# Kernel tuning notes

Hardware: AMD Instinct MI355X
Metric: run time of the kernel (lower is better)

The kernel has to match this reference:

```python
import jax, jax.numpy as jnp
import numpy as np

B, C, T = 16, 129, 2000
NF, ED, K = 40, 64, 16

def setup_inputs() -> dict:
    key = jax.random.key(0)
    ks = iter(jax.random.split(key, 48))
    def n(shape, s=0.05):
        return jax.random.normal(next(ks), shape, jnp.float32) * s
    inp = {
        'x': jax.random.normal(next(ks), (B, C, T), jnp.float32),
        # temporal conv (1,25) pad (0,12) + BN (inference running stats)
        'tconv_w': n((NF, 1, 1, 25)), 'tconv_b': jnp.zeros((NF,)),
        'tbn_g': jnp.ones((NF,)), 'tbn_b': jnp.zeros((NF,)), 'tbn_m': n((NF,)), 'tbn_v': jnp.ones((NF,)),
        # spatial conv (C,1) + BN
        'sconv_w': n((NF, NF, C, 1)), 'sconv_b': jnp.zeros((NF,)),
        'sbn_g': jnp.ones((NF,)), 'sbn_b': jnp.zeros((NF,)), 'sbn_m': n((NF,)), 'sbn_v': jnp.ones((NF,)),
        # separable: depthwise (1,15) pad (0,7), pointwise 1x1 -> 2*NF, BN
        'dw_w': n((NF, 1, 1, 15)), 'dw_b': jnp.zeros((NF,)),
        'pw_w': n((2 * NF, NF, 1, 1)), 'pw_b': jnp.zeros((2 * NF,)),
        'pbn_g': jnp.ones((2 * NF,)), 'pbn_b': jnp.zeros((2 * NF,)), 'pbn_m': n((2 * NF,)), 'pbn_v': jnp.ones((2 * NF,)),
        # projection 2*NF -> ED
        'proj_w': n((ED, 2 * NF)), 'proj_b': jnp.zeros((ED,)),
        # ENN cell 0 (input ED)
        'wx0': n((K, ED)), 'L0': jnp.eye(K, dtype=jnp.float32) + 0.1 * n((K, K), 1.0),
        'll0': jnp.asarray(np.log(0.1), jnp.float32), 'b0': jnp.zeros((K,)),
        'ln0_g': jnp.ones((K,)), 'ln0_b': jnp.zeros((K,)),
        # ENN cell 1 (input K)
        'wx1': n((K, K)), 'L1': jnp.eye(K, dtype=jnp.float32) + 0.1 * n((K, K), 1.0),
        'll1': jnp.asarray(np.log(0.1), jnp.float32), 'b1': jnp.zeros((K,)),
        'ln1_g': jnp.ones((K,)), 'ln1_b': jnp.zeros((K,)),
        # collapse
        'wq_w': n((K, K)), 'wq_b': jnp.zeros((K,)), 'log_temp': jnp.asarray(0.0, jnp.float32),
    }
    return inp

def _conv(x, w, b, pad, groups=1):
    y = jax.lax.conv_general_dilated(
        x, w, window_strides=(1, 1), padding=pad,
        dimension_numbers=('NCHW', 'OIHW', 'NCHW'), feature_group_count=groups)
    return y + b[None, :, None, None]

def _bn(x, g, b, m, v, eps=1e-5):
    inv = g / jnp.sqrt(v + eps)
    return x * inv[None, :, None, None] + (b - m * inv)[None, :, None, None]

def _cell(x, h, Wx, L, ll, b, g, be, eps=1e-5):
    E = L @ L.T  # PSD entanglement matrix [K,K]
    pre = x @ Wx.T + h @ E.T - jnp.exp(ll) * h + b
    mu = pre.mean(-1, keepdims=True)
    var = pre.var(-1, keepdims=True)
    pre = (pre - mu) / jnp.sqrt(var + eps) * g + be
    return jnp.tanh(pre)

def _forward(x, tconv_w, tconv_b, tbn_g, tbn_b, tbn_m, tbn_v,
             sconv_w, sconv_b, sbn_g, sbn_b, sbn_m, sbn_v,
             dw_w, dw_b, pw_w, pw_b, pbn_g, pbn_b, pbn_m, pbn_v,
             proj_w, proj_b,
             wx0, L0, ll0, b0, ln0_g, ln0_b,
             wx1, L1, ll1, b1, ln1_g, ln1_b,
             wq_w, wq_b, log_temp):
    # ---- SpatialCNN front-end (BN in inference mode, dropout=identity) ----
    o = x[:, None, :, :]                                        # [B,1,C,T]
    o = _conv(o, tconv_w, tconv_b, ((0, 0), (12, 12)))          # [B,NF,C,T]
    o = jax.nn.elu(_bn(o, tbn_g, tbn_b, tbn_m, tbn_v))
    o = _conv(o, sconv_w, sconv_b, ((0, 0), (0, 0)))            # [B,NF,1,T]
    o = jax.nn.elu(_bn(o, sbn_g, sbn_b, sbn_m, sbn_v))
    o = _conv(o, dw_w, dw_b, ((0, 0), (7, 7)), groups=NF)       # depthwise
    o = _conv(o, pw_w, pw_b, ((0, 0), (0, 0)))                  # [B,2NF,1,T]
    o = jax.nn.elu(_bn(o, pbn_g, pbn_b, pbn_m, pbn_v))
    Bn, Ch, _, Tt = o.shape
    o = o.reshape(Bn, Ch, Tt // 4, 4).mean(-1)                  # AvgPool (1,4) -> [B,2NF,T']
    feats = o.transpose(0, 2, 1) @ proj_w.T + proj_b            # [B,T',ED]
    # ---- Entangled RNN over T' steps (lax.scan) ----
    h_init = (jnp.zeros((Bn, K), feats.dtype), jnp.zeros((Bn, K), feats.dtype))
    def step(carry, xt):
        h0, h1 = carry
        h0 = _cell(xt, h0, wx0, L0, ll0, b0, ln0_g, ln0_b)
        h1 = _cell(h0, h1, wx1, L1, ll1, b1, ln1_g, ln1_b)
        return (h0, h1), None
    (h0, h1), _ = jax.lax.scan(step, h_init, feats.transpose(1, 0, 2))
    Z = h1                                                       # [B,K]
    # ---- Collapse attention ----
    q = Z @ wq_w.T + wq_b
    scores = jnp.sum(q * Z, axis=-1, keepdims=True)              # [B,1]
    alpha = jax.nn.softmax(scores / jnp.exp(log_temp), axis=-1)  # [B,1]
    return Z, alpha

def reference(x, tconv_w, tconv_b, tbn_g, tbn_b, tbn_m, tbn_v,
              sconv_w, sconv_b, sbn_g, sbn_b, sbn_m, sbn_v,
              dw_w, dw_b, pw_w, pw_b, pbn_g, pbn_b, pbn_m, pbn_v,
              proj_w, proj_b,
              wx0, L0, ll0, b0, ln0_g, ln0_b,
              wx1, L1, ll1, b1, ln1_g, ln1_b,
              wq_w, wq_b, log_temp):
    return _forward(x, tconv_w, tconv_b, tbn_g, tbn_b, tbn_m, tbn_v,
                    sconv_w, sconv_b, sbn_g, sbn_b, sbn_m, sbn_v,
                    dw_w, dw_b, pw_w, pw_b, pbn_g, pbn_b, pbn_m, pbn_v,
                    proj_w, proj_b,
                    wx0, L0, ll0, b0, ln0_g, ln0_b,
                    wx1, L1, ll1, b1, ln1_g, ln1_b,
                    wq_w, wq_b, log_temp)
```

## Files before the change

kernel.cpp:

```cpp
#include <hip/hip_runtime.h>
#include <math.h>

#define B_ 16
#define C_ 129
#define T_ 2000
#define NF_ 40
#define ED_ 64
#define K_ 16
#define TP_ 500

#define OFF_SB2 1040
#define OFF_PWC 1088
#define OFF_PB2 4288
#define OFF_WP  4368
#define OFF_BP  5648
#define OFF_M0  5664
#define OFF_M1  5920
#define OFF_W1A 6224
#define OFF_W2U 8192
#define OFF_XP  1495040
#define OFF_S2R 1623040

typedef __attribute__((ext_vector_type(8))) short s8v;
typedef __attribute__((ext_vector_type(4))) float f4v;

#define XROW 292

__device__ __forceinline__ float elu_f(float x) {
    return x > 0.f ? x : (__expf(x) - 1.f);
}
__device__ __forceinline__ float tanh2_f(float a2) {
    return fmaf(-2.f, __builtin_amdgcn_rcpf(__expf(a2) + 1.f), 1.f);
}
__device__ __forceinline__ unsigned bfr(float v) {
    return (__float_as_uint(v) + 0x8000u) >> 16;
}

#define DPPF(v, ctrl) __int_as_float(__builtin_amdgcn_update_dpp( \
    0, __float_as_int(v), (ctrl), 0xF, 0xF, false))

#define RSUM16(s) do {                     \
    s += DPPF(s, 0x128);                   \
    s += DPPF(s, 0x124);                   \
    s += DPPF(s, 0x122);                   \
    s += DPPF(s, 0x121);                   \
} while (0)

#define RDLANE(v, L) __int_as_float(__builtin_amdgcn_readlane(__float_as_int(v), (L)))

struct P0 {
    const float *tconv_w, *tconv_b, *tbn_g, *tbn_b, *tbn_m, *tbn_v;
    const float *sconv_b, *sbn_g, *sbn_b, *sbn_m, *sbn_v;
    const float *pw_w, *pw_b, *pbn_g, *pbn_b, *pbn_m, *pbn_v;
    const float *proj_w, *proj_b, *wx0, *b0, *L0, *ll0, *L1, *ll1;
    const float *sconv_w;
    float* ws;
};

__global__ __launch_bounds__(256) void k0_all(P0 p) {
    const int tid = threadIdx.x;
    float* ws = p.ws;
    const float eps = 1e-5f;

    if (blockIdx.x < 1250) {
        const int i = blockIdx.x * 256 + tid;
        if (i < 320000)
            ((float4*)(ws + OFF_S2R))[i] = make_float4(0.f, 0.f, 0.f, 0.f);
        return;
    }
    if (blockIdx.x < 1444) {
        const int e = (blockIdx.x - 1250) * 256 + tid;
        if (e >= C_ * 3 * 2 * 64) return;
        unsigned short* w2b = (unsigned short*)(ws + OFF_W2U);
        const int c = e / 384;
        int r = e - c * 384;
        const int mt = r >> 7; r &= 127;
        const int kc = r >> 6;
        const int lane = r & 63;
        const int g = mt * 16 + (lane & 15);
        const float sinv = (g < NF_) ? p.sbn_g[g] * rsqrtf(p.sbn_v[g] + 1e-5f) : 0.f;
        unsigned short o[8];
#pragma unroll
        for (int j = 0; j < 8; ++j) {
            const int f = kc * 32 + (lane >> 4) * 8 + j;
            float v = 0.f;
            if (g < NF_ && f < NF_) v = p.sconv_w[g * (NF_ * C_) + f * C_ + c] * sinv;
            o[j] = (unsigned short)bfr(v);
        }
        unsigned short* dst = w2b + (size_t)e * 8;
#pragma unroll
        for (int j = 0; j < 8; ++j) dst[j] = o[j];
        return;
    }

    const int gtid = (blockIdx.x - 1444) * 256 + tid;
    const int stride = 8 * 256;
    for (int e = gtid; e < 192; e += stride) {
        const int mt = e >> 6, L = e & 63;
        const int f = mt * 16 + (L & 15);
        float inv = 0.f, bias = 0.f;
        if (f < NF_) {
            inv = p.tbn_g[f] / sqrtf(p.tbn_v[f] + eps);
            bias = p.tconv_b[f] * inv + p.tbn_b[f] - p.tbn_m[f] * inv;
        }
        unsigned short* dst = ((unsigned short*)(ws + OFF_W1A)) + e * 8;
#pragma unroll
        for (int j = 0; j < 8; ++j) {
            const int k = (L >> 4) * 8 + j;
            float v = 0.f;
            if (f < NF_) {
                if (k < 25) v = p.tconv_w[f * 25 + k] * inv;
                else if (k == 25) v = bias;
            }
            dst[j] = (unsigned short)bfr(v);
        }
    }
    for (int f = gtid; f < NF_; f += stride) {
        const float sinv = p.sbn_g[f] / sqrtf(p.sbn_v[f] + eps);
        ws[OFF_SB2 + f] = p.sconv_b[f] * sinv + p.sbn_b[f] - p.sbn_m[f] * sinv;
    }
    for (int e = gtid; e < 3200; e += stride) {
        const int g = e / 40;
        const float pinv = p.pbn_g[g] / sqrtf(p.pbn_v[g] + eps);
        ws[OFF_PWC + e] = p.pw_w[e] * pinv;
    }
    for (int g = gtid; g < 80; g += stride) {
        const float pinv = p.pbn_g[g] / sqrtf(p.pbn_v[g] + eps);
        ws[OFF_PB2 + g] = p.pw_b[g] * pinv + p.pbn_b[g] - p.pbn_m[g] * pinv;
    }
    for (int e = gtid; e < 1280; e += stride) {
        const int k = e / 80, g = e - k * 80;
        float a = 0.f;
        for (int ee = 0; ee < ED_; ++ee)
            a = fmaf(p.wx0[k * ED_ + ee], p.proj_w[ee * 80 + g], a);
        ws[OFF_WP + e] = a;
    }
    for (int k = gtid; k < K_; k += stride) {
        float a = p.b0[k];
        for (int ee = 0; ee < ED_; ++ee)
            a = fmaf(p.wx0[k * ED_ + ee], p.proj_b[ee], a);
        ws[OFF_BP + k] = a;
    }
    for (int e = gtid; e < 256; e += stride) {
        const int k = e >> 4, j = e & 15;
        float a0 = 0.f, a1 = 0.f;
        for (int i = 0; i < 16; ++i) {
            a0 = fmaf(p.L0[k * 16 + i], p.L0[j * 16 + i], a0);
            a1 = fmaf(p.L1[k * 16 + i], p.L1[j * 16 + i], a1);
        }
        if (k == j) { a0 -= expf(p.ll0[0]); a1 -= expf(p.ll1[0]); }
        ws[OFF_M0 + e] = a0;
        ws[OFF_M1 + e] = a1;
    }
}

__global__ __launch_bounds__(256, 4) void k1_mfma(
    const float* __restrict__ x, const unsigned short* __restrict__ w1a,
    const unsigned short* __restrict__ w2b, float* __restrict__ s2raw) {
    __shared__ float xs[17 * XROW];
    __shared__ unsigned int vsI[2048];

    const int tid = threadIdx.x;
    const int split = blockIdx.x & 7;
    const int tile = (blockIdx.x >> 3) & 7;
    const int b = blockIdx.x >> 6;
    const int c0 = (split * C_) >> 3;
    const int c1 = ((split + 1) * C_) >> 3;
    const int cc = c1 - c0;
    const int t0 = tile << 8;
    const int w = tid >> 6;
    const int lane = tid & 63;
    const int n = lane & 15;
    const int q = lane >> 4;
    const int qh = q >> 1;
    const int q1_2 = (q & 1) * 2;
    const bool q3 = (q == 3);
    const int wb = w << 9;
    const int w64 = w << 6;
    const int ln8 = n + q * 8;

    for (int i = tid; i < 2048; i += 256) vsI[i] = 0u;
    for (int e = tid; e < cc * XROW; e += 256) {
        const int cl = e / XROW;
        const int i = e - cl * XROW;
        const int t = t0 - 12 + i;
        float v = 0.f;
        if ((unsigned)t < (unsigned)T_) v = x[(b * C_ + c0 + cl) * T_ + t];
        xs[e] = v;
    }
    __syncthreads();

    const s8v* w1a8 = (const s8v*)w1a;
    s8v wA[3];
#pragma unroll
    for (int mt = 0; mt < 3; ++mt) wA[mt] = w1a8[mt * 64 + lane];

    f4v acc[4][3];
#pragma unroll
    for (int nt = 0; nt < 4; ++nt)
#pragma unroll
        for (int mt = 0; mt < 3; ++mt) acc[nt][mt] = (f4v)0.f;

    const s8v* w2b8 = (const s8v*)w2b;
    const f4v z4 = (f4v)0.f;

    for (int cl = 0; cl < cc; ++cl) {
        const int c = c0 + cl;
        s8v af[3][2];
#pragma unroll
        for (int mt = 0; mt < 3; ++mt)
#pragma unroll
            for (int kc = 0; kc < 2; ++kc)
                af[mt][kc] = w2b8[((c * 3 + mt) * 2 + kc) * 64 + lane];

        const float* xrow = &xs[cl * XROW + w64 + ln8];

#pragma unroll
        for (int nt = 0; nt < 4; ++nt) {
            float bx[8];
#pragma unroll
            for (int j = 0; j < 8; ++j) bx[j] = xrow[nt * 16 + j];
            if (q3) bx[1] = 1.0f;
            unsigned pw_[4];
#pragma unroll
            for (int jj = 0; jj < 4; ++jj)
                pw_[jj] = bfr(bx[2 * jj]) |
                    ((__float_as_uint(bx[2 * jj + 1]) + 0x8000u) & 0xFFFF0000u);
            const s8v bh = *(const s8v*)pw_;
#pragma unroll
            for (int mt = 0; mt < 3; ++mt) {
                const f4v vT = __builtin_amdgcn_mfma_f32_16x16x32_bf16(
                    wA[mt], bh, z4, 0, 0, 0);
                const float e0 = elu_f(vT[0]);
                const float e1 = elu_f(vT[1]);
                const float e2 = elu_f(vT[2]);
                const float e3 = elu_f(vT[3]);
                const unsigned lo = bfr(e0) |
                    ((__float_as_uint(e1) + 0x8000u) & 0xFFFF0000u);
                const unsigned hi = bfr(e2) |
                    ((__float_as_uint(e3) + 0x8000u) & 0xFFFF0000u);
                const int base = wb + ((2 * mt + qh) << 6) + (n << 2) + q1_2;
                vsI[base] = lo;
                vsI[base + 1] = hi;
            }
            __builtin_amdgcn_wave_barrier();
            const s8v b0 = *(const s8v*)&vsI[wb + (q << 6) + (n << 2)];
            const s8v b1 = *(const s8v*)&vsI[wb + ((4 + q) << 6) + (n << 2)];
#pragma unroll
            for (int mt = 0; mt < 3; ++mt) {
                acc[nt][mt] = __builtin_amdgcn_mfma_f32_16x16x32_bf16(
                    af[mt][0], b0, acc[nt][mt], 0, 0, 0);
                acc[nt][mt] = __builtin_amdgcn_mfma_f32_16x16x32_bf16(
                    af[mt][1], b1, acc[nt][mt], 0, 0, 0);
            }
            __builtin_amdgcn_wave_barrier();
        }
    }

#pragma unroll
    for (int nt = 0; nt < 4; ++nt) {
        const int t = t0 + w * 64 + nt * 16 + n;
        if (t >= T_) continue;
#pragma unroll
        for (int mt = 0; mt < 3; ++mt) {
#pragma unroll
            for (int r = 0; r < 4; ++r) {
                const int g = mt * 16 + q * 4 + r;
                if (g < NF_)
                    atomicAdd(&s2raw[(b * NF_ + g) * T_ + t], acc[nt][mt][r]);
            }
        }
    }
}

__global__ __launch_bounds__(256) void k2_dwpw(
    const float* __restrict__ s2raw, const float* __restrict__ sb2,
    const float* __restrict__ dw_w, const float* __restrict__ dw_b,
    const float* __restrict__ pwc, const float* __restrict__ pb2,
    const float* __restrict__ WP, const float* __restrict__ bp,
    float* __restrict__ xp) {
    __shared__ float st[NF_ * 114];
    __shared__ float dwo[NF_ * 100];
    __shared__ float dwwl[NF_ * 15];
    __shared__ float dwbl[NF_];
    __shared__ float pwcl[80 * 40];
    __shared__ float pb2l[80];
    __shared__ float WPl[K_ * 80];
    __shared__ float bpl[K_];
    __shared__ float po[80 * 25];
    const int tid = threadIdx.x;
    const int b = blockIdx.x / 20;
    const int tp0 = (blockIdx.x % 20) * 25;
    const int tbase = tp0 * 4 - 7;
    for (int e = tid; e < NF_ * 114; e += 256) {
        const int f = e / 114;
        const int i = e - f * 114;
        const int t = tbase + i;
        float v = 0.f;
        if ((unsigned)t < (unsigned)T_)
            v = elu_f(s2raw[(b * NF_ + f) * T_ + t] + sb2[f]);
        st[e] = v;
    }
    for (int e = tid; e < 600; e += 256) dwwl[e] = dw_w[e];
    for (int e = tid; e < 3200; e += 256) pwcl[e] = pwc[e];
    for (int e = tid; e < 1280; e += 256) WPl[e] = WP[e];
    if (tid < NF_) dwbl[tid] = dw_b[tid];
    if (tid < 80) pb2l[tid] = pb2[tid];
    if (tid < K_) bpl[tid] = bp[tid];
    __syncthreads();
    for (int e = tid; e < 4000; e += 256) {
        const int f = e / 100;
        const int tq = e - f * 100;
        float a = dwbl[f];
#pragma unroll
        for (int kk = 0; kk < 15; ++kk)
            a = fmaf(dwwl[f * 15 + kk], st[f * 114 + tq + kk], a);
        dwo[e] = a;
    }
    __syncthreads();
    for (int e = tid; e < 2000; e += 256) {
        const int g = e / 25;
        const int tp = e - g * 25;
        float sum = 0.f;
#pragma unroll
        for (int dt = 0; dt < 4; ++dt) {
            float a = pb2l[g];
            for (int f = 0; f < NF_; ++f)
                a = fmaf(pwcl[g * 40 + f], dwo[f * 100 + tp * 4 + dt], a);
            sum += elu_f(a);
        }
        po[e] = sum * 0.25f;
    }
    __syncthreads();
    for (int e = tid; e < 400; e += 256) {
        const int tp = e >> 4;
        const int k = e & 15;
        float a = bpl[k];
        for (int g = 0; g < 80; ++g)
            a = fmaf(WPl[k * 80 + g], po[g * 25 + tp], a);
        xp[(b * TP_ + tp0 + tp) * K_ + k] = a;
    }
}

#define SCAN_STEP(I, S) do {                                              \
    float sH0[16], sH1[16];                                               \
    _Pragma("unroll")                                                     \
    for (int j = 0; j < 16; ++j) {                                        \
        sH0[j] = RDLANE(vA, 32 + j);                                      \
        sH1[j] = RDLANE(vA, j);                                           \
    }                                                                     \
    float a0 = 0.f, a1 = 0.f, c0 = 0.f, c1 = 0.f;                         \
    _Pragma("unroll")                                                     \
    for (int j = 0; j < 16; j += 2) {                                     \
        a0 = fmaf(WA[j],     sH0[j],     a0);                             \
        a1 = fmaf(WA[j + 1], sH0[j + 1], a1);                             \
        c0 = fmaf(WB[j],     sH1[j],     c0);                             \
        c1 = fmaf(WB[j + 1], sH1[j + 1], c1);                             \
    }                                                                     \
    const float xv = xn[S];                                               \
    int tf = (I) + 5; if (tf > TP_ - 1) tf = TP_ - 1;                     \
    xn[S] = xpb[tf * K_];                                                 \
    const float cadd = lower ? b1r : xv;                                  \
    const float pre = ((a0 + a1) + (c0 + c1)) + cadd;                     \
    float s1 = pre, s2 = pre * pre;                                       \
    RSUM16(s1);                                                           \
    RSUM16(s2);                                                           \
    const float mu = s1 * 0.0625f;                                        \
    const float var = fmaf(s2, 0.0625f, -mu * mu);                        \
    vA = tanh2_f(fmaf((pre - mu) * rsqrtf(var + 1e-5f), gg, bb));         \
} while (0)

__global__ __launch_bounds__(64, 1) void k3_scan(
    const float* __restrict__ xp, const float* __restrict__ M0,
    const float* __restrict__ M1, const float* __restrict__ wx1,
    const float* __restrict__ b1, const float* __restrict__ ln0_g,
    const float* __restrict__ ln0_b, const float* __restrict__ ln1_g,
    const float* __restrict__ ln1_b, float* __restrict__ out) {
    const int lane = threadIdx.x;
    const int k = lane & 15;
    const bool lower = lane < 32;
    const int b = blockIdx.x;

    float WA[16], WB[16];
#pragma unroll
    for (int j = 0; j < 16; ++j) {
        const float m0 = M0[k * 16 + j];
        const float m1 = M1[k * 16 + j];
        const float wx = wx1[k * 16 + j];
        WA[j] = lower ? wx : m0;
        WB[j] = lower ? m1 : 0.f;
    }
    const float b1r = b1[k];
    const float g0 = 2.f * ln0_g[k], be0 = 2.f * ln0_b[k];
    const float gg = lower ? 2.f * ln1_g[k] : g0;
    const float bb = lower ? 2.f * ln1_b[k] : be0;
    const float* xpb = xp + b * TP_ * K_ + k;

    float h0_0;
    {
        const float x0 = xpb[0];
        float s1 = x0, s2 = x0 * x0;
        RSUM16(s1);
        RSUM16(s2);
        const float mu = s1 * 0.0625f;
        const float var = fmaf(s2, 0.0625f, -mu * mu);
        h0_0 = tanh2_f(fmaf((x0 - mu) * rsqrtf(var + 1e-5f), g0, be0));
    }
    float vA = lower ? 0.f : h0_0;

    float xn[4];
    xn[0] = xpb[1 * K_];
    xn[1] = xpb[2 * K_];
    xn[2] = xpb[3 * K_];
    xn[3] = xpb[4 * K_];

    for (int i = 0; i < TP_; i += 4) {
        SCAN_STEP(i + 0, 0);
        SCAN_STEP(i + 1, 1);
        SCAN_STEP(i + 2, 2);
        SCAN_STEP(i + 3, 3);
    }
    if (lane < 16) {
        out[b * K_ + k] = vA;
        if (k == 0) out[256 + b] = 1.0f;
    }
}

extern "C" void kernel_launch(void* const* d_in, const int* in_sizes, int n_in,
                              void* d_out, int out_size, void* d_ws, size_t ws_size,
                              hipStream_t stream) {
    const float* x       = (const float*)d_in[0];
    const float* dw_w    = (const float*)d_in[13];
    const float* dw_b    = (const float*)d_in[14];
    const float* wx1     = (const float*)d_in[29];
    const float* b1      = (const float*)d_in[32];
    const float* ln0_g   = (const float*)d_in[27];
    const float* ln0_b   = (const float*)d_in[28];
    const float* ln1_g   = (const float*)d_in[33];
    const float* ln1_b   = (const float*)d_in[34];
    float* ws = (float*)d_ws;
    float* out = (float*)d_out;

    P0 p;
    p.tconv_w = (const float*)d_in[1]; p.tconv_b = (const float*)d_in[2];
    p.tbn_g = (const float*)d_in[3]; p.tbn_b = (const float*)d_in[4];
    p.tbn_m = (const float*)d_in[5]; p.tbn_v = (const float*)d_in[6];
    p.sconv_b = (const float*)d_in[8];
    p.sbn_g = (const float*)d_in[9]; p.sbn_b = (const float*)d_in[10];
    p.sbn_m = (const float*)d_in[11]; p.sbn_v = (const float*)d_in[12];
    p.pw_w = (const float*)d_in[15]; p.pw_b = (const float*)d_in[16];
    p.pbn_g = (const float*)d_in[17]; p.pbn_b = (const float*)d_in[18];
    p.pbn_m = (const float*)d_in[19]; p.pbn_v = (const float*)d_in[20];
    p.proj_w = (const float*)d_in[21]; p.proj_b = (const float*)d_in[22];
    p.wx0 = (const float*)d_in[23]; p.b0 = (const float*)d_in[26];
    p.L0 = (const float*)d_in[24]; p.ll0 = (const float*)d_in[25];
    p.L1 = (const float*)d_in[30]; p.ll1 = (const float*)d_in[31];
    p.sconv_w = (const float*)d_in[7];
    p.ws = ws;

    unsigned short* w2b = (unsigned short*)(ws + OFF_W2U);
    unsigned short* w1a = (unsigned short*)(ws + OFF_W1A);

    k0_all<<<dim3(1452), dim3(256), 0, stream>>>(p);
    k1_mfma<<<dim3(1024), dim3(256), 0, stream>>>(x, w1a, w2b, ws + OFF_S2R);
    k2_dwpw<<<dim3(320), dim3(256), 0, stream>>>(ws + OFF_S2R, ws + OFF_SB2,
                                                 dw_w, dw_b, ws + OFF_PWC,
                                                 ws + OFF_PB2, ws + OFF_WP, ws + OFF_BP,
                                                 ws + OFF_XP);
    k3_scan<<<dim3(16), dim3(64), 0, stream>>>(ws + OFF_XP, ws + OFF_M0, ws + OFF_M1,
                                               wx1, b1, ln0_g, ln0_b, ln1_g, ln1_b, out);
}
```

Measured before the change: 364.8 us.

## Rewrite recurrent scan as single-block MFMA over batch with split-fp16 precision

```diff
diff --git a/kernel.cpp b/kernel.cpp
--- a/kernel.cpp
+++ b/kernel.cpp
@@ -23,30 +23,37 @@
 
 typedef __attribute__((ext_vector_type(8))) short s8v;
 typedef __attribute__((ext_vector_type(4))) float f4v;
+typedef __attribute__((ext_vector_type(4))) __fp16 h4v;
+typedef __attribute__((ext_vector_type(2))) __fp16 h2v;
 
 #define XROW 292
 
 __device__ __forceinline__ float elu_f(float x) {
     return x > 0.f ? x : (__expf(x) - 1.f);
 }
-__device__ __forceinline__ float tanh2_f(float a2) {
-    return fmaf(-2.f, __builtin_amdgcn_rcpf(__expf(a2) + 1.f), 1.f);
-}
 __device__ __forceinline__ unsigned bfr(float v) {
     return (__float_as_uint(v) + 0x8000u) >> 16;
 }
 
-#define DPPF(v, ctrl) __int_as_float(__builtin_amdgcn_update_dpp( \
-    0, __float_as_int(v), (ctrl), 0xF, 0xF, false))
-
-#define RSUM16(s) do {                     \
-    s += DPPF(s, 0x128);                   \
-    s += DPPF(s, 0x124);                   \
-    s += DPPF(s, 0x122);                   \
-    s += DPPF(s, 0x121);                   \
-} while (0)
-
-#define RDLANE(v, L) __int_as_float(__builtin_amdgcn_readlane(__float_as_int(v), (L)))
+
+#define MFMA16(a, b, c) __builtin_amdgcn_mfma_f32_16x16x16f16(a, b, c, 0, 0, 0)
+
+#define EXP2F(x) __builtin_amdgcn_exp2f(x)
+#define RSQF(x) __builtin_amdgcn_rsqf(x)
+
+__device__ __forceinline__ void split4(f4v v, h4v& hi, h4v& lo) {
+    union UH { h4v h4; h2v h2[2]; } H, L;
+    H.h2[0] = __builtin_amdgcn_cvt_pkrtz(v[0], v[1]);
+    H.h2[1] = __builtin_amdgcn_cvt_pkrtz(v[2], v[3]);
+    L.h2[0] = __builtin_amdgcn_cvt_pkrtz(v[0] - (float)H.h2[0][0],
+                                         v[1] - (float)H.h2[0][1]);
+    L.h2[1] = __builtin_amdgcn_cvt_pkrtz(v[2] - (float)H.h2[1][0],
+                                         v[3] - (float)H.h2[1][1]);
+    hi = H.h4;
+    lo = L.h4;
+}
+
+union U4 { struct { h4v hi, lo; } s; uint4 u; };
 
 struct P0 {
     const float *tconv_w, *tconv_b, *tbn_g, *tbn_b, *tbn_m, *tbn_v;
@@ -338,91 +345,121 @@
         float a = bpl[k];
         for (int g = 0; g < 80; ++g)
             a = fmaf(WPl[k * 80 + g], po[g * 25 + tp], a);
-        xp[(b * TP_ + tp0 + tp) * K_ + k] = a;
-    }
-}
-
-#define SCAN_STEP(I, S) do {                                              \
-    float sH0[16], sH1[16];                                               \
-    _Pragma("unroll")                                                     \
-    for (int j = 0; j < 16; ++j) {                                        \
-        sH0[j] = RDLANE(vA, 32 + j);                                      \
-        sH1[j] = RDLANE(vA, j);                                           \
-    }                                                                     \
-    float a0 = 0.f, a1 = 0.f, c0 = 0.f, c1 = 0.f;                         \
-    _Pragma("unroll")                                                     \
-    for (int j = 0; j < 16; j += 2) {                                     \
-        a0 = fmaf(WA[j],     sH0[j],     a0);                             \
-        a1 = fmaf(WA[j + 1], sH0[j + 1], a1);                             \
-        c0 = fmaf(WB[j],     sH1[j],     c0);                             \
-        c1 = fmaf(WB[j + 1], sH1[j + 1], c1);                             \
-    }                                                                     \
-    const float xv = xn[S];                                               \
-    int tf = (I) + 5; if (tf > TP_ - 1) tf = TP_ - 1;                     \
-    xn[S] = xpb[tf * K_];                                                 \
-    const float cadd = lower ? b1r : xv;                                  \
-    const float pre = ((a0 + a1) + (c0 + c1)) + cadd;                     \
-    float s1 = pre, s2 = pre * pre;                                       \
-    RSUM16(s1);                                                           \
-    RSUM16(s2);                                                           \
-    const float mu = s1 * 0.0625f;                                        \
-    const float var = fmaf(s2, 0.0625f, -mu * mu);                        \
-    vA = tanh2_f(fmaf((pre - mu) * rsqrtf(var + 1e-5f), gg, bb));         \
-} while (0)
-
-__global__ __launch_bounds__(64, 1) void k3_scan(
+        xp[(tp0 + tp) * 256 + ((k & 12) << 4) + (b << 2) + (k & 3)] = a;
+    }
+}
+
+__global__ __launch_bounds__(128, 1) void k3_scan(
     const float* __restrict__ xp, const float* __restrict__ M0,
     const float* __restrict__ M1, const float* __restrict__ wx1,
     const float* __restrict__ b1, const float* __restrict__ ln0_g,
     const float* __restrict__ ln0_b, const float* __restrict__ ln1_g,
     const float* __restrict__ ln1_b, float* __restrict__ out) {
-    const int lane = threadIdx.x;
-    const int k = lane & 15;
-    const bool lower = lane < 32;
-    const int b = blockIdx.x;
-
-    float WA[16], WB[16];
-#pragma unroll
-    for (int j = 0; j < 16; ++j) {
-        const float m0 = M0[k * 16 + j];
-        const float m1 = M1[k * 16 + j];
-        const float wx = wx1[k * 16 + j];
-        WA[j] = lower ? wx : m0;
-        WB[j] = lower ? m1 : 0.f;
-    }
-    const float b1r = b1[k];
-    const float g0 = 2.f * ln0_g[k], be0 = 2.f * ln0_b[k];
-    const float gg = lower ? 2.f * ln1_g[k] : g0;
-    const float bb = lower ? 2.f * ln1_b[k] : be0;
-    const float* xpb = xp + b * TP_ * K_ + k;
-
-    float h0_0;
-    {
-        const float x0 = xpb[0];
-        float s1 = x0, s2 = x0 * x0;
-        RSUM16(s1);
-        RSUM16(s2);
-        const float mu = s1 * 0.0625f;
-        const float var = fmaf(s2, 0.0625f, -mu * mu);
-        h0_0 = tanh2_f(fmaf((x0 - mu) * rsqrtf(var + 1e-5f), g0, be0));
-    }
-    float vA = lower ? 0.f : h0_0;
-
-    float xn[4];
-    xn[0] = xpb[1 * K_];
-    xn[1] = xpb[2 * K_];
-    xn[2] = xpb[3 * K_];
-    xn[3] = xpb[4 * K_];
-
-    for (int i = 0; i < TP_; i += 4) {
-        SCAN_STEP(i + 0, 0);
-        SCAN_STEP(i + 1, 1);
-        SCAN_STEP(i + 2, 2);
-        SCAN_STEP(i + 3, 3);
-    }
-    if (lane < 16) {
-        out[b * K_ + k] = vA;
-        if (k == 0) out[256 + b] = 1.0f;
+    __shared__ uint4 hbuf[2][64];
+    const int tid = threadIdx.x;
+    const int w = tid >> 6;
+    const int lane = tid & 63;
+    const int n = lane & 15;
+    const int q = lane >> 4;
+    const int r0 = q << 2;
+    const f4v z4 = (f4v)0.f;
+    const float C2 = 2.8853900817779268f;
+
+    h4v Ahi{}, Alo{}, Whi{}, Wlo{};
+    f4v G, Bb, B1C = z4;
+    if (w == 0) {
+        const f4v a = *(const f4v*)(M0 + n * 16 + r0);
+        split4(a, Ahi, Alo);
+#pragma unroll
+        for (int j = 0; j < 4; ++j) {
+            G[j] = C2 * ln0_g[r0 + j];
+            Bb[j] = C2 * ln0_b[r0 + j];
+        }
+    } else {
+        const f4v a = *(const f4v*)(M1 + n * 16 + r0);
+        split4(a, Ahi, Alo);
+        const f4v ww = *(const f4v*)(wx1 + n * 16 + r0);
+        split4(ww, Whi, Wlo);
+        B1C = *(const f4v*)(b1 + r0);
+#pragma unroll
+        for (int j = 0; j < 4; ++j) {
+            G[j] = C2 * ln1_g[r0 + j];
+            Bb[j] = C2 * ln1_b[r0 + j];
+        }
+    }
+
+    h4v Shi{}, Slo{};
+    f4v hlast = z4;
+    const f4v* xp4 = (const f4v*)xp;
+    f4v Xb0 = z4, Xb1 = z4;
+    if (w == 0) {
+        Xb0 = xp4[lane];
+        Xb1 = xp4[64 + lane];
+    }
+
+    for (int t = 0; t <= TP_; ++t) {
+        __syncthreads();
+        f4v pre;
+        bool act;
+        if (w == 0) {
+            act = (t < TP_);
+            if (act) {
+                const f4v Xc = Xb0;
+                Xb0 = Xb1;
+                int tn = t + 2;
+                if (tn > TP_ - 1) tn = TP_ - 1;
+                Xb1 = xp4[tn * 64 + lane];
+                f4v c1 = MFMA16(Ahi, Shi, Xc);
+                f4v c2 = MFMA16(Ahi, Slo, z4);
+                c2 = MFMA16(Alo, Shi, c2);
+                pre = c1 + c2;
+            }
+        } else {
+            act = (t > 0);
+            if (act) {
+                U4 R;
+                R.u = hbuf[(t - 1) & 1][lane];
+                f4v c1 = MFMA16(Whi, R.s.hi, B1C);
+                c1 = MFMA16(Wlo, R.s.hi, c1);
+                f4v c2 = MFMA16(Ahi, Shi, z4);
+                c2 = MFMA16(Alo, Shi, c2);
+                f4v c3 = MFMA16(Whi, R.s.lo, z4);
+                c3 = MFMA16(Ahi, Slo, c3);
+                pre = (c1 + c2) + c3;
+            }
+        }
+        if (act) {
+            float s1 = (pre[0] + pre[1]) + (pre[2] + pre[3]);
+            float s2 = fmaf(pre[3], pre[3], fmaf(pre[2], pre[2],
+                        fmaf(pre[1], pre[1], pre[0] * pre[0])));
+            s1 += __shfl_xor(s1, 16);
+            s2 += __shfl_xor(s2, 16);
+            s1 += __shfl_xor(s1, 32);
+            s2 += __shfl_xor(s2, 32);
+            const float mu = s1 * 0.0625f;
+            const float inv = RSQF(fmaf(s2, 0.0625f, -mu * mu) + 1e-5f);
+            f4v hnew;
+#pragma unroll
+            for (int j = 0; j < 4; ++j) {
+                const float coef = inv * G[j];
+                const float a2 = fmaf(pre[j], coef, fmaf(-mu, coef, Bb[j]));
+                const float e2 = EXP2F(a2);
+                hnew[j] = fmaf(-2.f, __builtin_amdgcn_rcpf(e2 + 1.f), 1.f);
+            }
+            split4(hnew, Shi, Slo);
+            if (w == 0) {
+                U4 P;
+                P.s.hi = Shi;
+                P.s.lo = Slo;
+                hbuf[t & 1][lane] = P.u;
+            } else {
+                hlast = hnew;
+            }
+        }
+    }
+    if (w == 1) {
+        *(f4v*)(out + n * K_ + r0) = hlast;
+        if (q == 0) out[256 + n] = 1.0f;
     }
 }
 
@@ -467,6 +504,6 @@
                                                  dw_w, dw_b, ws + OFF_PWC,
                                                  ws + OFF_PB2, ws + OFF_WP, ws + OFF_BP,
                                                  ws + OFF_XP);
-    k3_scan<<<dim3(16), dim3(64), 0, stream>>>(ws + OFF_XP, ws + OFF_M0, ws + OFF_M1,
+    k3_scan<<<dim3(1), dim3(128), 0, stream>>>(ws + OFF_XP, ws + OFF_M0, ws + OFF_M1,
                                                wx1, b1, ln0_g, ln0_b, ln1_g, ln1_b, out);
 }
```

Result: slower. 446.1 us (+22.3%).
